# Optimization experiments

Hardware: AMD Instinct MI355X
Metric: run time of the kernel (lower is better)

## Reference

```python
import jax, jax.numpy as jnp
import numpy as np

N = 100000
E = 1600000
D_IN = 64
D_HID = 64
D_OUT = 64
R = 8
BN_EPS = 1e-5


def setup_inputs() -> dict:
    key = jax.random.key(0)
    ks = jax.random.split(key, 12)
    x = jax.random.normal(ks[0], (N, D_IN), dtype=jnp.float32)
    edge_index = jax.random.randint(ks[1], (2, E), 0, N, dtype=jnp.int64)
    edge_type = jax.random.randint(ks[2], (E,), 0, R, dtype=jnp.int64)
    s1 = 1.0 / np.sqrt(D_IN)
    s2 = 1.0 / np.sqrt(D_HID)
    w1 = jax.random.uniform(ks[3], (R, D_IN, D_HID), jnp.float32, -s1, s1)
    root1 = jax.random.uniform(ks[4], (D_IN, D_HID), jnp.float32, -s1, s1)
    b1 = jnp.zeros((D_HID,), jnp.float32)
    gamma1 = jnp.ones((D_HID,), jnp.float32)
    beta1 = jnp.zeros((D_HID,), jnp.float32)
    w2 = jax.random.uniform(ks[5], (R, D_HID, D_OUT), jnp.float32, -s2, s2)
    root2 = jax.random.uniform(ks[6], (D_HID, D_OUT), jnp.float32, -s2, s2)
    b2 = jnp.zeros((D_OUT,), jnp.float32)
    return {"x": x, "edge_index": edge_index, "edge_type": edge_type,
            "w1": w1, "root1": root1, "b1": b1, "gamma1": gamma1, "beta1": beta1,
            "w2": w2, "root2": root2, "b2": b2}


def rgcn_conv(x, edge_index, edge_type, W, root, bias):
    # PyG RGCNConv with aggr='mean': per relation r, mean of neighbor features
    # over incoming edges of type r, transformed by W[r]; plus root transform + bias.
    # Aggregate-then-transform (legal since transform is linear): one fused
    # segment_sum keyed by (dst, relation), then a grouped GEMM via einsum.
    n, d = x.shape
    src, dst = edge_index[0], edge_index[1]
    seg = dst * R + edge_type                     # [E] combined segment id
    msg = x[src]                                  # [E, d] gather
    agg = jax.ops.segment_sum(msg, seg, num_segments=n * R).reshape(n, R, d)
    cnt = jax.ops.segment_sum(jnp.ones((src.shape[0],), x.dtype), seg,
                              num_segments=n * R).reshape(n, R, 1)
    mean = agg / jnp.maximum(cnt, 1.0)            # [n, R, d]
    return jnp.einsum('nrd,rdo->no', mean, W) + x @ root + bias


def batch_norm(h, gamma, beta):
    mu = h.mean(axis=0)
    var = h.var(axis=0)
    return gamma * (h - mu) * jax.lax.rsqrt(var + BN_EPS) + beta


def reference(x, edge_index, edge_type, w1, root1, b1, gamma1, beta1, w2, root2, b2):
    h = rgcn_conv(x, edge_index, edge_type, w1, root1, b1)
    h = jax.nn.relu(batch_norm(h, gamma1, beta1))
    # dropout: identity (eval mode)
    out = rgcn_conv(h, edge_index, edge_type, w2, root2, b2)
    return out
```

## Files before the change

kernel.cpp:

```cpp
#include <hip/hip_runtime.h>
#include <hip/hip_bf16.h>

#define NN 100000
#define EE 1600000
#define RR 8
#define DD 64
#define MM (NN * RR)
#define BN_EPS 1e-5f
#define KTOT 576
#define BSTRIDE 584

#define NB 391
#define EPB 8192
#define NBIN ((EE + EPB - 1) / EPB)

typedef __bf16 bf16x8 __attribute__((ext_vector_type(8)));
typedef float  f32x4  __attribute__((ext_vector_type(4)));

static __device__ __forceinline__ unsigned short f32_to_bf16(float f) {
    unsigned int u = __float_as_uint(f);
    unsigned int r = u + 0x7FFFu + ((u >> 16) & 1u);
    return (unsigned short)(r >> 16);
}
static __device__ __forceinline__ float bflo(unsigned int u) {
    return __uint_as_float(u << 16);
}
static __device__ __forceinline__ float bfhi(unsigned int u) {
    return __uint_as_float(u & 0xFFFF0000u);
}


__global__ void k_bcount(const int* __restrict__ dst, int* __restrict__ btot) {
    __shared__ int cnt[NB];
    int t = threadIdx.x;
    for (int i = t; i < NB; i += 256) cnt[i] = 0;
    __syncthreads();
    int base = blockIdx.x * EPB;
#pragma unroll
    for (int i = 0; i < EPB / 256; ++i) {
        int e = base + i * 256 + t;
        if (e < EE) atomicAdd(&cnt[dst[e] >> 8], 1);
    }
    __syncthreads();
    for (int i = t; i < NB; i += 256)
        if (cnt[i]) atomicAdd(&btot[i], cnt[i]);
}

__global__ void k_bscan(const int* __restrict__ btot, int* __restrict__ bbase,
                        int* __restrict__ gcur, int* __restrict__ rowptr) {
    __shared__ int sd[512];
    int t = threadIdx.x;
    int v = (t < NB) ? btot[t] : 0;
    sd[t] = v;
    __syncthreads();
    for (int off = 1; off < 512; off <<= 1) {
        int x = (t >= off) ? sd[t - off] : 0;
        __syncthreads();
        sd[t] += x;
        __syncthreads();
    }
    if (t < NB) { bbase[t] = sd[t] - v; gcur[t] = sd[t] - v; }
    if (t == NB - 1) { bbase[NB] = sd[t]; rowptr[MM] = sd[t]; }
}

__global__ void k_bin(const int* __restrict__ src, const int* __restrict__ dst,
                      const int* __restrict__ et, int* __restrict__ gcur,
                      unsigned int* __restrict__ ebuf) {
    __shared__ int cnt[NB];
    __shared__ int bas[NB];
    __shared__ int off[NB];
    int t = threadIdx.x;
    for (int i = t; i < NB; i += 256) { cnt[i] = 0; off[i] = 0; }
    __syncthreads();
    int base = blockIdx.x * EPB;
#pragma unroll
    for (int i = 0; i < EPB / 256; ++i) {
        int e = base + i * 256 + t;
        if (e < EE) atomicAdd(&cnt[dst[e] >> 8], 1);
    }
    __syncthreads();
    for (int i = t; i < NB; i += 256) {
        int c = cnt[i];
        bas[i] = c ? atomicAdd(&gcur[i], c) : 0;
    }
    __syncthreads();
#pragma unroll
    for (int i = 0; i < EPB / 256; ++i) {
        int e = base + i * 256 + t;
        if (e < EE) {
            int d = dst[e];
            int b = d >> 8;
            int lk = ((d & 255) << 3) | et[e];
            unsigned int rec0 = (unsigned int)src[e] | ((unsigned int)lk << 17);
            int p = bas[b] + atomicAdd(&off[b], 1);
            ebuf[p] = rec0;
        }
    }
}

__global__ __launch_bounds__(256) void k_bcsr(const int* __restrict__ bbase,
                                              const unsigned int* __restrict__ ebuf,
                                              int* __restrict__ rowptr,
                                              int* __restrict__ rec) {
    __shared__ int deg[2048];
    __shared__ int part[256];
    int b = blockIdx.x, t = threadIdx.x;
    int e0 = bbase[b], e1 = bbase[b + 1];
    for (int i = t; i < 2048; i += 256) deg[i] = 0;
    __syncthreads();
    for (int e = e0 + t; e < e1; e += 256) atomicAdd(&deg[ebuf[e] >> 17], 1);
    __syncthreads();
    int loc[8];
    int s = 0;
#pragma unroll
    for (int j = 0; j < 8; ++j) { loc[j] = deg[t * 8 + j]; s += loc[j]; }
    part[t] = s;
    __syncthreads();
    for (int off = 1; off < 256; off <<= 1) {
        int x = (t >= off) ? part[t - off] : 0;
        __syncthreads();
        part[t] += x;
        __syncthreads();
    }
    int run = part[t] - s;
    int keyBase = b * 2048;
#pragma unroll
    for (int j = 0; j < 8; ++j) {
        int g = keyBase + t * 8 + j;
        if (g < MM) rowptr[g] = e0 + run;
        deg[t * 8 + j] = run;
        run += loc[j];
    }
    __syncthreads();
    for (int e = e0 + t; e < e1; e += 256) {
        unsigned int v = ebuf[e];
        int lk = v >> 17;
        int pos = e0 + atomicAdd(&deg[lk], 1);
        rec[pos] = (int)(v & 0x1FFFFu);
    }
}


__global__ void k_tobf16(const float* __restrict__ X, unsigned short* __restrict__ Xb) {
    int i = blockIdx.x * 256 + threadIdx.x;
    if (i >= NN * DD / 4) return;
    float4 v = ((const float4*)X)[i];
    ushort4 o;
    o.x = f32_to_bf16(v.x); o.y = f32_to_bf16(v.y);
    o.z = f32_to_bf16(v.z); o.w = f32_to_bf16(v.w);
    ((ushort4*)Xb)[i] = o;
}


__global__ void k_agg(const unsigned short* __restrict__ Xb,
                      const int* __restrict__ rowptr,
                      const int* __restrict__ rec,
                      unsigned short* __restrict__ mean) {
    int wv = threadIdx.x >> 6;
    int lane = threadIdx.x & 63;
    int n = blockIdx.x * 4 + wv;
    if (n >= NN) return;
    int r = lane >> 3;
    int q = lane & 7;
    int e0 = rowptr[n * RR + r];
    int e1 = rowptr[n * RR + r + 1];
    float a0[8] = {0,0,0,0,0,0,0,0};
    float a1[8] = {0,0,0,0,0,0,0,0};
    float a2[8] = {0,0,0,0,0,0,0,0};
    float a3[8] = {0,0,0,0,0,0,0,0};
    int e = e0;
    for (; e + 3 < e1; e += 4) {
        int s0 = rec[e], s1 = rec[e + 1], s2 = rec[e + 2], s3 = rec[e + 3];
        uint4 u0 = *(const uint4*)(Xb + (size_t)s0 * DD + q * 8);
        uint4 u1 = *(const uint4*)(Xb + (size_t)s1 * DD + q * 8);
        uint4 u2 = *(const uint4*)(Xb + (size_t)s2 * DD + q * 8);
        uint4 u3 = *(const uint4*)(Xb + (size_t)s3 * DD + q * 8);
        a0[0] += bflo(u0.x); a0[1] += bfhi(u0.x); a0[2] += bflo(u0.y); a0[3] += bfhi(u0.y);
        a0[4] += bflo(u0.z); a0[5] += bfhi(u0.z); a0[6] += bflo(u0.w); a0[7] += bfhi(u0.w);
        a1[0] += bflo(u1.x); a1[1] += bfhi(u1.x); a1[2] += bflo(u1.y); a1[3] += bfhi(u1.y);
        a1[4] += bflo(u1.z); a1[5] += bfhi(u1.z); a1[6] += bflo(u1.w); a1[7] += bfhi(u1.w);
        a2[0] += bflo(u2.x); a2[1] += bfhi(u2.x); a2[2] += bflo(u2.y); a2[3] += bfhi(u2.y);
        a2[4] += bflo(u2.z); a2[5] += bfhi(u2.z); a2[6] += bflo(u2.w); a2[7] += bfhi(u2.w);
        a3[0] += bflo(u3.x); a3[1] += bfhi(u3.x); a3[2] += bflo(u3.y); a3[3] += bfhi(u3.y);
        a3[4] += bflo(u3.z); a3[5] += bfhi(u3.z); a3[6] += bflo(u3.w); a3[7] += bfhi(u3.w);
    }
    if (e + 1 < e1) {
        int s0 = rec[e], s1 = rec[e + 1];
        uint4 u0 = *(const uint4*)(Xb + (size_t)s0 * DD + q * 8);
        uint4 u1 = *(const uint4*)(Xb + (size_t)s1 * DD + q * 8);
        a0[0] += bflo(u0.x); a0[1] += bfhi(u0.x); a0[2] += bflo(u0.y); a0[3] += bfhi(u0.y);
        a0[4] += bflo(u0.z); a0[5] += bfhi(u0.z); a0[6] += bflo(u0.w); a0[7] += bfhi(u0.w);
        a1[0] += bflo(u1.x); a1[1] += bfhi(u1.x); a1[2] += bflo(u1.y); a1[3] += bfhi(u1.y);
        a1[4] += bflo(u1.z); a1[5] += bfhi(u1.z); a1[6] += bflo(u1.w); a1[7] += bfhi(u1.w);
        e += 2;
    }
    if (e < e1) {
        int s0 = rec[e];
        uint4 u0 = *(const uint4*)(Xb + (size_t)s0 * DD + q * 8);
        a0[0] += bflo(u0.x); a0[1] += bfhi(u0.x); a0[2] += bflo(u0.y); a0[3] += bfhi(u0.y);
        a0[4] += bflo(u0.z); a0[5] += bfhi(u0.z); a0[6] += bflo(u0.w); a0[7] += bfhi(u0.w);
    }
    int cnt = e1 - e0;
    float inv = 1.0f / (float)(cnt > 1 ? cnt : 1);
    uint4 o;
    o.x = (unsigned)f32_to_bf16((a0[0]+a1[0]+a2[0]+a3[0]) * inv) | ((unsigned)f32_to_bf16((a0[1]+a1[1]+a2[1]+a3[1]) * inv) << 16);
    o.y = (unsigned)f32_to_bf16((a0[2]+a1[2]+a2[2]+a3[2]) * inv) | ((unsigned)f32_to_bf16((a0[3]+a1[3]+a2[3]+a3[3]) * inv) << 16);
    o.z = (unsigned)f32_to_bf16((a0[4]+a1[4]+a2[4]+a3[4]) * inv) | ((unsigned)f32_to_bf16((a0[5]+a1[5]+a2[5]+a3[5]) * inv) << 16);
    o.w = (unsigned)f32_to_bf16((a0[6]+a1[6]+a2[6]+a3[6]) * inv) | ((unsigned)f32_to_bf16((a0[7]+a1[7]+a2[7]+a3[7]) * inv) << 16);
    *(uint4*)(mean + (size_t)n * 512 + r * 64 + q * 8) = o;
}


__global__ void k_prepw(const float* __restrict__ W, const float* __restrict__ Root,
                        unsigned short* __restrict__ WcT) {
    int i = blockIdx.x * 256 + threadIdx.x;
    if (i >= 64 * KTOT) return;
    int o = i / KTOT;
    int k = i - o * KTOT;
    float v;
    if (k < 512) v = W[(size_t)(k >> 6) * 4096 + (k & 63) * 64 + o];
    else         v = Root[(k - 512) * 64 + o];
    WcT[(size_t)o * KTOT + k] = f32_to_bf16(v);
}


__global__ __launch_bounds__(256) void k_gemm(const unsigned short* __restrict__ meanB,
                                              const unsigned short* __restrict__ Xb,
                                              const unsigned short* __restrict__ WcT,
                                              const float* __restrict__ bias,
                                              float* __restrict__ Out,
                                              float* __restrict__ stats,
                                              int dostats) {
    __shared__ unsigned short Bs[64 * BSTRIDE];
    __shared__ float ssum[4][64];
    __shared__ float ssq[4][64];
    int t = threadIdx.x;
#pragma unroll
    for (int i = 0; i < 18; ++i) {
        int idx = i * 256 + t;
        int row = idx / 72;
        int k16 = idx - row * 72;
        uint4 v = *(const uint4*)(WcT + (size_t)row * KTOT + k16 * 8);
        *(uint4*)(Bs + row * BSTRIDE + k16 * 8) = v;
    }
    __syncthreads();

    int wv = t >> 6, lane = t & 63;
    int quad = lane >> 4, m16 = lane & 15;
    int row0 = blockIdx.x * 128 + wv * 32;
    int r0 = row0 + m16;
    int r1 = row0 + 16 + m16;
    bool ok0 = r0 < NN, ok1 = r1 < NN;

    union AU { uint4 u; bf16x8 f; };
    f32x4 acc[2][4];
#pragma unroll
    for (int i = 0; i < 2; ++i)
#pragma unroll
        for (int j = 0; j < 4; ++j) acc[i][j] = (f32x4){0.f, 0.f, 0.f, 0.f};

    const unsigned short* a0p = meanB + (size_t)r0 * 512 + quad * 8;
    const unsigned short* a1p = meanB + (size_t)r1 * 512 + quad * 8;
    const unsigned short* x0p = Xb + (size_t)r0 * DD + quad * 8;
    const unsigned short* x1p = Xb + (size_t)r1 * DD + quad * 8;
    const unsigned short* bs  = Bs + m16 * BSTRIDE + quad * 8;

#pragma unroll
    for (int kb = 0; kb < 16; ++kb) {
        AU av0, av1, bv[4];
        if (ok0) av0.u = *(const uint4*)(a0p + kb * 32); else av0.u = make_uint4(0,0,0,0);
        if (ok1) av1.u = *(const uint4*)(a1p + kb * 32); else av1.u = make_uint4(0,0,0,0);
#pragma unroll
        for (int nt = 0; nt < 4; ++nt)
            bv[nt].u = *(const uint4*)(bs + nt * 16 * BSTRIDE + kb * 32);
#pragma unroll
        for (int nt = 0; nt < 4; ++nt) {
            acc[0][nt] = __builtin_amdgcn_mfma_f32_16x16x32_bf16(av0.f, bv[nt].f, acc[0][nt], 0, 0, 0);
            acc[1][nt] = __builtin_amdgcn_mfma_f32_16x16x32_bf16(av1.f, bv[nt].f, acc[1][nt], 0, 0, 0);
        }
    }
#pragma unroll
    for (int kb = 0; kb < 2; ++kb) {
        AU av0, av1, bv[4];
        if (ok0) av0.u = *(const uint4*)(x0p + kb * 32); else av0.u = make_uint4(0,0,0,0);
        if (ok1) av1.u = *(const uint4*)(x1p + kb * 32); else av1.u = make_uint4(0,0,0,0);
#pragma unroll
        for (int nt = 0; nt < 4; ++nt)
            bv[nt].u = *(const uint4*)(bs + nt * 16 * BSTRIDE + 512 + kb * 32);
#pragma unroll
        for (int nt = 0; nt < 4; ++nt) {
            acc[0][nt] = __builtin_amdgcn_mfma_f32_16x16x32_bf16(av0.f, bv[nt].f, acc[0][nt], 0, 0, 0);
            acc[1][nt] = __builtin_amdgcn_mfma_f32_16x16x32_bf16(av1.f, bv[nt].f, acc[1][nt], 0, 0, 0);
        }
    }

#pragma unroll
    for (int rt = 0; rt < 2; ++rt) {
#pragma unroll
        for (int nt = 0; nt < 4; ++nt) {
            int col = nt * 16 + m16;
            float bb = bias[col];
#pragma unroll
            for (int i = 0; i < 4; ++i) {
                int row = row0 + rt * 16 + quad * 4 + i;
                if (row < NN) Out[(size_t)row * 64 + col] = acc[rt][nt][i] + bb;
            }
        }
    }

    if (dostats) {
#pragma unroll
        for (int nt = 0; nt < 4; ++nt) {
            int col = nt * 16 + m16;
            float bb = bias[col];
            float s = 0.f, sq = 0.f;
#pragma unroll
            for (int rt = 0; rt < 2; ++rt) {
#pragma unroll
                for (int i = 0; i < 4; ++i) {
                    int row = row0 + rt * 16 + quad * 4 + i;
                    if (row < NN) {
                        float v = acc[rt][nt][i] + bb;
                        s += v; sq += v * v;
                    }
                }
            }
            s += __shfl_xor(s, 16); s += __shfl_xor(s, 32);
            sq += __shfl_xor(sq, 16); sq += __shfl_xor(sq, 32);
            if (quad == 0) { ssum[wv][col] = s; ssq[wv][col] = sq; }
        }
        __syncthreads();
        if (t < 128) {
            int col = t & 63;
            if (t < 64) {
                float s = ssum[0][col] + ssum[1][col] + ssum[2][col] + ssum[3][col];
                atomicAdd(&stats[col], s);
            } else {
                float sq = ssq[0][col] + ssq[1][col] + ssq[2][col] + ssq[3][col];
                atomicAdd(&stats[64 + col], sq);
            }
        }
    }
}


__global__ void k_bnrelu(float* __restrict__ H, unsigned short* __restrict__ Hb,
                         const float* __restrict__ stats,
                         const float* __restrict__ gamma, const float* __restrict__ beta) {
    int idx = blockIdx.x * 256 + threadIdx.x;
    const int total = NN * DD / 4;
    if (idx >= total) return;
    int c0 = (idx & 15) * 4;
    float4 v = ((const float4*)H)[idx];
    float inv = 1.0f / (float)NN;
    float4 o;
    {
        float mu = stats[c0 + 0] * inv;
        float var = stats[64 + c0 + 0] * inv - mu * mu;
        float sc = gamma[c0 + 0] * rsqrtf(var + BN_EPS);
        float r = sc * (v.x - mu) + beta[c0 + 0];
        o.x = r > 0.f ? r : 0.f;
    }
    {
        float mu = stats[c0 + 1] * inv;
        float var = stats[64 + c0 + 1] * inv - mu * mu;
        float sc = gamma[c0 + 1] * rsqrtf(var + BN_EPS);
        float r = sc * (v.y - mu) + beta[c0 + 1];
        o.y = r > 0.f ? r : 0.f;
    }
    {
        float mu = stats[c0 + 2] * inv;
        float var = stats[64 + c0 + 2] * inv - mu * mu;
        float sc = gamma[c0 + 2] * rsqrtf(var + BN_EPS);
        float r = sc * (v.z - mu) + beta[c0 + 2];
        o.z = r > 0.f ? r : 0.f;
    }
    {
        float mu = stats[c0 + 3] * inv;
        float var = stats[64 + c0 + 3] * inv - mu * mu;
        float sc = gamma[c0 + 3] * rsqrtf(var + BN_EPS);
        float r = sc * (v.w - mu) + beta[c0 + 3];
        o.w = r > 0.f ? r : 0.f;
    }
    ((float4*)H)[idx] = o;
    ushort4 ob;
    ob.x = f32_to_bf16(o.x); ob.y = f32_to_bf16(o.y);
    ob.z = f32_to_bf16(o.z); ob.w = f32_to_bf16(o.w);
    ((ushort4*)Hb)[idx] = ob;
}


static inline size_t alignup(size_t x) { return (x + 255) & ~(size_t)255; }

extern "C" void kernel_launch(void* const* d_in, const int* in_sizes, int n_in,
                              void* d_out, int out_size, void* d_ws, size_t ws_size,
                              hipStream_t stream) {
    const float* x      = (const float*)d_in[0];
    const int*   eidx   = (const int*)d_in[1];
    const int*   etype  = (const int*)d_in[2];
    const float* w1     = (const float*)d_in[3];
    const float* root1  = (const float*)d_in[4];
    const float* b1     = (const float*)d_in[5];
    const float* gamma1 = (const float*)d_in[6];
    const float* beta1  = (const float*)d_in[7];
    const float* w2     = (const float*)d_in[8];
    const float* root2  = (const float*)d_in[9];
    const float* b2     = (const float*)d_in[10];
    float* out = (float*)d_out;

    const int* src = eidx;
    const int* dst = eidx + EE;

    char* w = (char*)d_ws;
    int* rowptr = (int*)w;            w += alignup((size_t)(MM + 1) * 4);
    int* btot   = (int*)w;            w += alignup(512 * 4);
    int* bbase  = (int*)w;            w += alignup(512 * 4);
    int* gcur   = (int*)w;            w += alignup(512 * 4);
    int* rec    = (int*)w;            w += alignup((size_t)EE * 4);
    unsigned short* mean = (unsigned short*)w; w += alignup((size_t)NN * 512 * 2);
    float* h    = (float*)w;          w += alignup((size_t)NN * DD * 4);
    unsigned short* xhb = (unsigned short*)w; w += alignup((size_t)NN * DD * 2);
    unsigned short* wct1 = (unsigned short*)w; w += alignup((size_t)64 * KTOT * 2);
    unsigned short* wct2 = (unsigned short*)w; w += alignup((size_t)64 * KTOT * 2);
    float* stats = (float*)w;         w += alignup(128 * 4);
    unsigned int* ebuf = (unsigned int*)mean;

    hipMemsetAsync(btot, 0, 512 * 4, stream);
    hipMemsetAsync(stats, 0, 128 * 4, stream);

    k_prepw<<<dim3(144), dim3(256), 0, stream>>>(w1, root1, wct1);
    k_prepw<<<dim3(144), dim3(256), 0, stream>>>(w2, root2, wct2);
    k_tobf16<<<dim3(NN * DD / 4 / 256 + 1), dim3(256), 0, stream>>>(x, xhb);

    k_bcount<<<dim3(NBIN), dim3(256), 0, stream>>>(dst, btot);
    k_bscan<<<dim3(1), dim3(512), 0, stream>>>(btot, bbase, gcur, rowptr);
    k_bin<<<dim3(NBIN), dim3(256), 0, stream>>>(src, dst, etype, gcur, ebuf);
    k_bcsr<<<dim3(NB), dim3(256), 0, stream>>>(bbase, ebuf, rowptr, rec);

    k_agg<<<dim3((NN + 3) / 4), dim3(256), 0, stream>>>(xhb, rowptr, rec, mean);
    k_gemm<<<dim3((NN + 127) / 128), dim3(256), 0, stream>>>(mean, xhb, wct1, b1, h, stats, 1);
    k_bnrelu<<<dim3(NN * DD / 4 / 256), dim3(256), 0, stream>>>(h, xhb, stats, gamma1, beta1);

    k_agg<<<dim3((NN + 3) / 4), dim3(256), 0, stream>>>(xhb, rowptr, rec, mean);
    k_gemm<<<dim3((NN + 127) / 128), dim3(256), 0, stream>>>(mean, xhb, wct2, b2, out, stats, 0);
}
```

Baseline: 377.4 us.

## Fuse neighbor aggregation into GEMM via shared-memory A tile

The separate aggregation kernel and GEMM kernel are merged into one kernel per layer. Each block aggregates 16 nodes' per-relation means plus the root features into a shared-memory A tile, then runs MFMA against weights read directly from global memory. This drops the 100000x512 bf16 mean buffer's write and read-back and one launch per layer. In exchange each block does only a small 16-row GEMM, B is loaded from global/L2 instead of LDS, and BN stats now use one atomic pair per wave per column, so there are many more atomics.

Result: slower. 476.1 us (+26.1%).

```diff
diff --git a/kernel.cpp b/kernel.cpp
--- a/kernel.cpp
+++ b/kernel.cpp
@@ -8,7 +8,7 @@
 #define MM (NN * RR)
 #define BN_EPS 1e-5f
 #define KTOT 576
-#define BSTRIDE 584
+#define APITCH 584
 
 #define NB 391
 #define EPB 8192
@@ -149,65 +149,6 @@
     o.x = f32_to_bf16(v.x); o.y = f32_to_bf16(v.y);
     o.z = f32_to_bf16(v.z); o.w = f32_to_bf16(v.w);
     ((ushort4*)Xb)[i] = o;
-}
-
-
-__global__ void k_agg(const unsigned short* __restrict__ Xb,
-                      const int* __restrict__ rowptr,
-                      const int* __restrict__ rec,
-                      unsigned short* __restrict__ mean) {
-    int wv = threadIdx.x >> 6;
-    int lane = threadIdx.x & 63;
-    int n = blockIdx.x * 4 + wv;
-    if (n >= NN) return;
-    int r = lane >> 3;
-    int q = lane & 7;
-    int e0 = rowptr[n * RR + r];
-    int e1 = rowptr[n * RR + r + 1];
-    float a0[8] = {0,0,0,0,0,0,0,0};
-    float a1[8] = {0,0,0,0,0,0,0,0};
-    float a2[8] = {0,0,0,0,0,0,0,0};
-    float a3[8] = {0,0,0,0,0,0,0,0};
-    int e = e0;
-    for (; e + 3 < e1; e += 4) {
-        int s0 = rec[e], s1 = rec[e + 1], s2 = rec[e + 2], s3 = rec[e + 3];
-        uint4 u0 = *(const uint4*)(Xb + (size_t)s0 * DD + q * 8);
-        uint4 u1 = *(const uint4*)(Xb + (size_t)s1 * DD + q * 8);
-        uint4 u2 = *(const uint4*)(Xb + (size_t)s2 * DD + q * 8);
-        uint4 u3 = *(const uint4*)(Xb + (size_t)s3 * DD + q * 8);
-        a0[0] += bflo(u0.x); a0[1] += bfhi(u0.x); a0[2] += bflo(u0.y); a0[3] += bfhi(u0.y);
-        a0[4] += bflo(u0.z); a0[5] += bfhi(u0.z); a0[6] += bflo(u0.w); a0[7] += bfhi(u0.w);
-        a1[0] += bflo(u1.x); a1[1] += bfhi(u1.x); a1[2] += bflo(u1.y); a1[3] += bfhi(u1.y);
-        a1[4] += bflo(u1.z); a1[5] += bfhi(u1.z); a1[6] += bflo(u1.w); a1[7] += bfhi(u1.w);
-        a2[0] += bflo(u2.x); a2[1] += bfhi(u2.x); a2[2] += bflo(u2.y); a2[3] += bfhi(u2.y);
-        a2[4] += bflo(u2.z); a2[5] += bfhi(u2.z); a2[6] += bflo(u2.w); a2[7] += bfhi(u2.w);
-        a3[0] += bflo(u3.x); a3[1] += bfhi(u3.x); a3[2] += bflo(u3.y); a3[3] += bfhi(u3.y);
-        a3[4] += bflo(u3.z); a3[5] += bfhi(u3.z); a3[6] += bflo(u3.w); a3[7] += bfhi(u3.w);
-    }
-    if (e + 1 < e1) {
-        int s0 = rec[e], s1 = rec[e + 1];
-        uint4 u0 = *(const uint4*)(Xb + (size_t)s0 * DD + q * 8);
-        uint4 u1 = *(const uint4*)(Xb + (size_t)s1 * DD + q * 8);
-        a0[0] += bflo(u0.x); a0[1] += bfhi(u0.x); a0[2] += bflo(u0.y); a0[3] += bfhi(u0.y);
-        a0[4] += bflo(u0.z); a0[5] += bfhi(u0.z); a0[6] += bflo(u0.w); a0[7] += bfhi(u0.w);
-        a1[0] += bflo(u1.x); a1[1] += bfhi(u1.x); a1[2] += bflo(u1.y); a1[3] += bfhi(u1.y);
-        a1[4] += bflo(u1.z); a1[5] += bfhi(u1.z); a1[6] += bflo(u1.w); a1[7] += bfhi(u1.w);
-        e += 2;
-    }
-    if (e < e1) {
-        int s0 = rec[e];
-        uint4 u0 = *(const uint4*)(Xb + (size_t)s0 * DD + q * 8);
-        a0[0] += bflo(u0.x); a0[1] += bfhi(u0.x); a0[2] += bflo(u0.y); a0[3] += bfhi(u0.y);
-        a0[4] += bflo(u0.z); a0[5] += bfhi(u0.z); a0[6] += bflo(u0.w); a0[7] += bfhi(u0.w);
-    }
-    int cnt = e1 - e0;
-    float inv = 1.0f / (float)(cnt > 1 ? cnt : 1);
-    uint4 o;
-    o.x = (unsigned)f32_to_bf16((a0[0]+a1[0]+a2[0]+a3[0]) * inv) | ((unsigned)f32_to_bf16((a0[1]+a1[1]+a2[1]+a3[1]) * inv) << 16);
-    o.y = (unsigned)f32_to_bf16((a0[2]+a1[2]+a2[2]+a3[2]) * inv) | ((unsigned)f32_to_bf16((a0[3]+a1[3]+a2[3]+a3[3]) * inv) << 16);
-    o.z = (unsigned)f32_to_bf16((a0[4]+a1[4]+a2[4]+a3[4]) * inv) | ((unsigned)f32_to_bf16((a0[5]+a1[5]+a2[5]+a3[5]) * inv) << 16);
-    o.w = (unsigned)f32_to_bf16((a0[6]+a1[6]+a2[6]+a3[6]) * inv) | ((unsigned)f32_to_bf16((a0[7]+a1[7]+a2[7]+a3[7]) * inv) << 16);
-    *(uint4*)(mean + (size_t)n * 512 + r * 64 + q * 8) = o;
 }
 
 
@@ -224,121 +165,107 @@
 }
 
 
-__global__ __launch_bounds__(256) void k_gemm(const unsigned short* __restrict__ meanB,
-                                              const unsigned short* __restrict__ Xb,
-                                              const unsigned short* __restrict__ WcT,
-                                              const float* __restrict__ bias,
-                                              float* __restrict__ Out,
-                                              float* __restrict__ stats,
-                                              int dostats) {
-    __shared__ unsigned short Bs[64 * BSTRIDE];
-    __shared__ float ssum[4][64];
-    __shared__ float ssq[4][64];
+__global__ __launch_bounds__(256) void k_aggemm(const unsigned short* __restrict__ Xb,
+                                                const int* __restrict__ rowptr,
+                                                const int* __restrict__ rec,
+                                                const unsigned short* __restrict__ WcT,
+                                                const float* __restrict__ bias,
+                                                float* __restrict__ Out,
+                                                float* __restrict__ stats,
+                                                int dostats) {
+    __shared__ unsigned short As[16 * APITCH];
     int t = threadIdx.x;
-#pragma unroll
-    for (int i = 0; i < 18; ++i) {
-        int idx = i * 256 + t;
-        int row = idx / 72;
-        int k16 = idx - row * 72;
-        uint4 v = *(const uint4*)(WcT + (size_t)row * KTOT + k16 * 8);
-        *(uint4*)(Bs + row * BSTRIDE + k16 * 8) = v;
-    }
-    __syncthreads();
-
     int wv = t >> 6, lane = t & 63;
+    int n0 = blockIdx.x * 16;
+    int r = lane >> 3;
+    int q = lane & 7;
+
+#pragma unroll 1
+    for (int j = 0; j < 4; ++j) {
+        int row = wv * 4 + j;
+        int n = n0 + row;
+        int e0 = rowptr[n * RR + r];
+        int e1 = rowptr[n * RR + r + 1];
+        float a0[8] = {0,0,0,0,0,0,0,0};
+        float a1[8] = {0,0,0,0,0,0,0,0};
+        float a2[8] = {0,0,0,0,0,0,0,0};
+        float a3[8] = {0,0,0,0,0,0,0,0};
+        int e = e0;
+        for (; e + 3 < e1; e += 4) {
+            int s0 = rec[e], s1 = rec[e + 1], s2 = rec[e + 2], s3 = rec[e + 3];
+            uint4 u0 = *(const uint4*)(Xb + (size_t)s0 * DD + q * 8);
+            uint4 u1 = *(const uint4*)(Xb + (size_t)s1 * DD + q * 8);
+            uint4 u2 = *(const uint4*)(Xb + (size_t)s2 * DD + q * 8);
+            uint4 u3 = *(const uint4*)(Xb + (size_t)s3 * DD + q * 8);
+            a0[0] += bflo(u0.x); a0[1] += bfhi(u0.x); a0[2] += bflo(u0.y); a0[3] += bfhi(u0.y);
+            a0[4] += bflo(u0.z); a0[5] += bfhi(u0.z); a0[6] += bflo(u0.w); a0[7] += bfhi(u0.w);
+            a1[0] += bflo(u1.x); a1[1] += bfhi(u1.x); a1[2] += bflo(u1.y); a1[3] += bfhi(u1.y);
+            a1[4] += bflo(u1.z); a1[5] += bfhi(u1.z); a1[6] += bflo(u1.w); a1[7] += bfhi(u1.w);
+            a2[0] += bflo(u2.x); a2[1] += bfhi(u2.x); a2[2] += bflo(u2.y); a2[3] += bfhi(u2.y);
+            a2[4] += bflo(u2.z); a2[5] += bfhi(u2.z); a2[6] += bflo(u2.w); a2[7] += bfhi(u2.w);
+            a3[0] += bflo(u3.x); a3[1] += bfhi(u3.x); a3[2] += bflo(u3.y); a3[3] += bfhi(u3.y);
+            a3[4] += bflo(u3.z); a3[5] += bfhi(u3.z); a3[6] += bflo(u3.w); a3[7] += bfhi(u3.w);
+        }
+        if (e + 1 < e1) {
+            int s0 = rec[e], s1 = rec[e + 1];
+            uint4 u0 = *(const uint4*)(Xb + (size_t)s0 * DD + q * 8);
+            uint4 u1 = *(const uint4*)(Xb + (size_t)s1 * DD + q * 8);
+            a0[0] += bflo(u0.x); a0[1] += bfhi(u0.x); a0[2] += bflo(u0.y); a0[3] += bfhi(u0.y);
+            a0[4] += bflo(u0.z); a0[5] += bfhi(u0.z); a0[6] += bflo(u0.w); a0[7] += bfhi(u0.w);
+            a1[0] += bflo(u1.x); a1[1] += bfhi(u1.x); a1[2] += bflo(u1.y); a1[3] += bfhi(u1.y);
+            a1[4] += bflo(u1.z); a1[5] += bfhi(u1.z); a1[6] += bflo(u1.w); a1[7] += bfhi(u1.w);
+            e += 2;
+        }
+        if (e < e1) {
+            int s0 = rec[e];
+            uint4 u0 = *(const uint4*)(Xb + (size_t)s0 * DD + q * 8);
+            a0[0] += bflo(u0.x); a0[1] += bfhi(u0.x); a0[2] += bflo(u0.y); a0[3] += bfhi(u0.y);
+            a0[4] += bflo(u0.z); a0[5] += bfhi(u0.z); a0[6] += bflo(u0.w); a0[7] += bfhi(u0.w);
+        }
+        int cnt = e1 - e0;
+        float inv = 1.0f / (float)(cnt > 1 ? cnt : 1);
+        uint4 o;
+        o.x = (unsigned)f32_to_bf16((a0[0]+a1[0]+a2[0]+a3[0]) * inv) | ((unsigned)f32_to_bf16((a0[1]+a1[1]+a2[1]+a3[1]) * inv) << 16);
+        o.y = (unsigned)f32_to_bf16((a0[2]+a1[2]+a2[2]+a3[2]) * inv) | ((unsigned)f32_to_bf16((a0[3]+a1[3]+a2[3]+a3[3]) * inv) << 16);
+        o.z = (unsigned)f32_to_bf16((a0[4]+a1[4]+a2[4]+a3[4]) * inv) | ((unsigned)f32_to_bf16((a0[5]+a1[5]+a2[5]+a3[5]) * inv) << 16);
+        o.w = (unsigned)f32_to_bf16((a0[6]+a1[6]+a2[6]+a3[6]) * inv) | ((unsigned)f32_to_bf16((a0[7]+a1[7]+a2[7]+a3[7]) * inv) << 16);
+        *(uint4*)(As + row * APITCH + r * 64 + q * 8) = o;
+        if (r == 0) {
+            uint4 xo = *(const uint4*)(Xb + (size_t)n * DD + q * 8);
+            *(uint4*)(As + row * APITCH + 512 + q * 8) = xo;
+        }
+    }
+    __syncthreads();
+
     int quad = lane >> 4, m16 = lane & 15;
-    int row0 = blockIdx.x * 128 + wv * 32;
-    int r0 = row0 + m16;
-    int r1 = row0 + 16 + m16;
-    bool ok0 = r0 < NN, ok1 = r1 < NN;
-
     union AU { uint4 u; bf16x8 f; };
-    f32x4 acc[2][4];
-#pragma unroll
-    for (int i = 0; i < 2; ++i)
-#pragma unroll
-        for (int j = 0; j < 4; ++j) acc[i][j] = (f32x4){0.f, 0.f, 0.f, 0.f};
-
-    const unsigned short* a0p = meanB + (size_t)r0 * 512 + quad * 8;
-    const unsigned short* a1p = meanB + (size_t)r1 * 512 + quad * 8;
-    const unsigned short* x0p = Xb + (size_t)r0 * DD + quad * 8;
-    const unsigned short* x1p = Xb + (size_t)r1 * DD + quad * 8;
-    const unsigned short* bs  = Bs + m16 * BSTRIDE + quad * 8;
-
-#pragma unroll
-    for (int kb = 0; kb < 16; ++kb) {
-        AU av0, av1, bv[4];
-        if (ok0) av0.u = *(const uint4*)(a0p + kb * 32); else av0.u = make_uint4(0,0,0,0);
-        if (ok1) av1.u = *(const uint4*)(a1p + kb * 32); else av1.u = make_uint4(0,0,0,0);
-#pragma unroll
-        for (int nt = 0; nt < 4; ++nt)
-            bv[nt].u = *(const uint4*)(bs + nt * 16 * BSTRIDE + kb * 32);
-#pragma unroll
-        for (int nt = 0; nt < 4; ++nt) {
-            acc[0][nt] = __builtin_amdgcn_mfma_f32_16x16x32_bf16(av0.f, bv[nt].f, acc[0][nt], 0, 0, 0);
-            acc[1][nt] = __builtin_amdgcn_mfma_f32_16x16x32_bf16(av1.f, bv[nt].f, acc[1][nt], 0, 0, 0);
-        }
-    }
-#pragma unroll
-    for (int kb = 0; kb < 2; ++kb) {
-        AU av0, av1, bv[4];
-        if (ok0) av0.u = *(const uint4*)(x0p + kb * 32); else av0.u = make_uint4(0,0,0,0);
-        if (ok1) av1.u = *(const uint4*)(x1p + kb * 32); else av1.u = make_uint4(0,0,0,0);
-#pragma unroll
-        for (int nt = 0; nt < 4; ++nt)
-            bv[nt].u = *(const uint4*)(bs + nt * 16 * BSTRIDE + 512 + kb * 32);
-#pragma unroll
-        for (int nt = 0; nt < 4; ++nt) {
-            acc[0][nt] = __builtin_amdgcn_mfma_f32_16x16x32_bf16(av0.f, bv[nt].f, acc[0][nt], 0, 0, 0);
-            acc[1][nt] = __builtin_amdgcn_mfma_f32_16x16x32_bf16(av1.f, bv[nt].f, acc[1][nt], 0, 0, 0);
-        }
-    }
-
-#pragma unroll
-    for (int rt = 0; rt < 2; ++rt) {
-#pragma unroll
-        for (int nt = 0; nt < 4; ++nt) {
-            int col = nt * 16 + m16;
-            float bb = bias[col];
-#pragma unroll
-            for (int i = 0; i < 4; ++i) {
-                int row = row0 + rt * 16 + quad * 4 + i;
-                if (row < NN) Out[(size_t)row * 64 + col] = acc[rt][nt][i] + bb;
-            }
-        }
-    }
-
+    f32x4 acc = {0.f, 0.f, 0.f, 0.f};
+    const unsigned short* ap = As + m16 * APITCH + quad * 8;
+    const unsigned short* wp = WcT + (size_t)(wv * 16 + m16) * KTOT + quad * 8;
+#pragma unroll
+    for (int kb = 0; kb < 18; ++kb) {
+        AU a, b;
+        a.u = *(const uint4*)(ap + kb * 32);
+        b.u = *(const uint4*)(wp + kb * 32);
+        acc = __builtin_amdgcn_mfma_f32_16x16x32_bf16(a.f, b.f, acc, 0, 0, 0);
+    }
+
+    int col = wv * 16 + m16;
+    float bb = bias[col];
+    float s = 0.f, sq = 0.f;
+#pragma unroll
+    for (int i = 0; i < 4; ++i) {
+        int row = quad * 4 + i;
+        float v = acc[i] + bb;
+        Out[(size_t)(n0 + row) * 64 + col] = v;
+        s += v; sq += v * v;
+    }
     if (dostats) {
-#pragma unroll
-        for (int nt = 0; nt < 4; ++nt) {
-            int col = nt * 16 + m16;
-            float bb = bias[col];
-            float s = 0.f, sq = 0.f;
-#pragma unroll
-            for (int rt = 0; rt < 2; ++rt) {
-#pragma unroll
-                for (int i = 0; i < 4; ++i) {
-                    int row = row0 + rt * 16 + quad * 4 + i;
-                    if (row < NN) {
-                        float v = acc[rt][nt][i] + bb;
-                        s += v; sq += v * v;
-                    }
-                }
-            }
-            s += __shfl_xor(s, 16); s += __shfl_xor(s, 32);
-            sq += __shfl_xor(sq, 16); sq += __shfl_xor(sq, 32);
-            if (quad == 0) { ssum[wv][col] = s; ssq[wv][col] = sq; }
-        }
-        __syncthreads();
-        if (t < 128) {
-            int col = t & 63;
-            if (t < 64) {
-                float s = ssum[0][col] + ssum[1][col] + ssum[2][col] + ssum[3][col];
-                atomicAdd(&stats[col], s);
-            } else {
-                float sq = ssq[0][col] + ssq[1][col] + ssq[2][col] + ssq[3][col];
-                atomicAdd(&stats[64 + col], sq);
-            }
+        s += __shfl_xor(s, 16); s += __shfl_xor(s, 32);
+        sq += __shfl_xor(sq, 16); sq += __shfl_xor(sq, 32);
+        if (quad == 0) {
+            atomicAdd(&stats[col], s);
+            atomicAdd(&stats[64 + col], sq);
         }
     }
 }
@@ -417,13 +344,12 @@
     int* bbase  = (int*)w;            w += alignup(512 * 4);
     int* gcur   = (int*)w;            w += alignup(512 * 4);
     int* rec    = (int*)w;            w += alignup((size_t)EE * 4);
-    unsigned short* mean = (unsigned short*)w; w += alignup((size_t)NN * 512 * 2);
+    unsigned int* ebuf = (unsigned int*)w; w += alignup((size_t)EE * 4);
     float* h    = (float*)w;          w += alignup((size_t)NN * DD * 4);
     unsigned short* xhb = (unsigned short*)w; w += alignup((size_t)NN * DD * 2);
     unsigned short* wct1 = (unsigned short*)w; w += alignup((size_t)64 * KTOT * 2);
     unsigned short* wct2 = (unsigned short*)w; w += alignup((size_t)64 * KTOT * 2);
     float* stats = (float*)w;         w += alignup(128 * 4);
-    unsigned int* ebuf = (unsigned int*)mean;
 
     hipMemsetAsync(btot, 0, 512 * 4, stream);
     hipMemsetAsync(stats, 0, 128 * 4, stream);
@@ -437,10 +363,8 @@
     k_bin<<<dim3(NBIN), dim3(256), 0, stream>>>(src, dst, etype, gcur, ebuf);
     k_bcsr<<<dim3(NB), dim3(256), 0, stream>>>(bbase, ebuf, rowptr, rec);
 
-    k_agg<<<dim3((NN + 3) / 4), dim3(256), 0, stream>>>(xhb, rowptr, rec, mean);
-    k_gemm<<<dim3((NN + 127) / 128), dim3(256), 0, stream>>>(mean, xhb, wct1, b1, h, stats, 1);
+    k_aggemm<<<dim3(NN / 16), dim3(256), 0, stream>>>(xhb, rowptr, rec, wct1, b1, h, stats, 1);
     k_bnrelu<<<dim3(NN * DD / 4 / 256), dim3(256), 0, stream>>>(h, xhb, stats, gamma1, beta1);
 
-    k_agg<<<dim3((NN + 3) / 4), dim3(256), 0, stream>>>(xhb, rowptr, rec, mean);
-    k_gemm<<<dim3((NN + 127) / 128), dim3(256), 0, stream>>>(mean, xhb, wct2, b2, out, stats, 0);
-}
+    k_aggemm<<<dim3(NN / 16), dim3(256), 0, stream>>>(xhb, rowptr, rec, wct2, b2, out, stats, 0);
+}
```
